# Kernel optimization log

Measured on AMD Instinct MI355X. Metric: run time of the kernel, lower is better.

The kernel has to match this reference:

```python
import jax, jax.numpy as jnp
import numpy as np

LN_EPS = 1e-5


def layer_norm(x, g, b):
    m = jnp.mean(x, axis=-1, keepdims=True)
    v = jnp.mean((x - m) ** 2, axis=-1, keepdims=True)
    return (x - m) * jax.lax.rsqrt(v + LN_EPS) * g + b


def setup_inputs() -> dict:
    key = jax.random.key(0)
    ks = jax.random.split(key, 8)
    B, S, D, C = 32, 512, 768, 25
    return {
        "bert_feature": jax.random.normal(ks[0], (B, S, D), dtype=jnp.float32),
        "output_encoder": jax.random.normal(ks[1], (B, S, D), dtype=jnp.float32),
        "cos_sim": jax.random.normal(ks[2], (B, S, C), dtype=jnp.float32),
        "decoder_embedding": jax.random.normal(ks[3], (B, C, D), dtype=jnp.float32),
        "labels": jax.random.randint(ks[4], (B, S), 0, C, dtype=jnp.int32),
        "ln_gamma": jnp.ones((D,), dtype=jnp.float32),
        "ln_beta": jnp.zeros((D,), dtype=jnp.float32),
        "W_add": jax.random.normal(ks[5], (D, C), dtype=jnp.float32) * 0.02,
        "b_add": jnp.zeros((C,), dtype=jnp.float32),
        "start_trans": jax.random.normal(ks[6], (C,), dtype=jnp.float32) * 0.1,
        "end_trans": jax.random.normal(ks[7], (C,), dtype=jnp.float32) * 0.1,
        "trans": jax.random.normal(jax.random.fold_in(key, 99), (C, C), dtype=jnp.float32) * 0.1,
    }


def crf_neg_log_likelihood(emissions, tags, start, end, trans):
    # emissions [B,S,C] (log-probs), tags [B,S]; no mask (all valid), torchcrf semantics
    B, S, C = emissions.shape
    b = jnp.arange(B)
    # numerator (gold path score)
    em_sc = jnp.take_along_axis(emissions, tags[:, :, None], axis=2)[..., 0].sum(axis=1)
    tr_sc = trans[tags[:, :-1], tags[:, 1:]].sum(axis=1)
    num = start[tags[:, 0]] + em_sc + tr_sc + end[tags[:, -1]]
    # partition function via forward algorithm (scan over time)
    def step(score, em_t):  # score [B,C]
        ns = jax.nn.logsumexp(score[:, :, None] + trans[None] + em_t[:, None, :], axis=1)
        return ns, None
    score0 = start[None] + emissions[:, 0]
    scoreT, _ = jax.lax.scan(step, score0, jnp.swapaxes(emissions[:, 1:], 0, 1))
    logZ = jax.nn.logsumexp(scoreT + end[None], axis=1)
    llh = num - logZ
    return llh.mean()  # reduction='mean'


def crf_decode(emissions, start, end, trans):
    # Viterbi; emissions [B,S,C]
    B, S, C = emissions.shape
    def vstep(score, em_t):
        cand = score[:, :, None] + trans[None]      # [B, prev, cur]
        best = jnp.max(cand, axis=1) + em_t
        idx = jnp.argmax(cand, axis=1)              # [B, cur] -> best prev tag
        return best, idx
    score0 = start[None] + emissions[:, 0]
    scoreT, hist = jax.lax.scan(vstep, score0, jnp.swapaxes(emissions[:, 1:], 0, 1))
    last = jnp.argmax(scoreT + end[None], axis=1)   # [B]
    def back(tag, h):
        prev = jnp.take_along_axis(h, tag[:, None], axis=1)[:, 0]
        return prev, prev
    _, prevs = jax.lax.scan(back, last, hist, reverse=True)
    return jnp.concatenate([prevs, last[None]], axis=0).T  # [B,S]


def reference(bert_feature, output_encoder, cos_sim, decoder_embedding, labels,
              ln_gamma, ln_beta, W_add, b_add, start_trans, end_trans, trans):
    # dropout is identity at eval time
    bf = layer_norm(bert_feature, ln_gamma, ln_beta)
    # prob_times_query: triple python loop == bmm(cos_sim, LN(decoder_embedding))
    # NOTE: original (faithfully) passes raw cos_sim, not its softmax.
    dec = layer_norm(decoder_embedding, ln_gamma, ln_beta)
    prob_query = jnp.einsum('bsc,bcd->bsd', cos_sim, dec)
    emb = layer_norm(bf + output_encoder + prob_query, ln_gamma, ln_beta)
    emb = jax.nn.relu(emb)
    ner_prob = jax.nn.log_softmax(emb @ W_add + b_add, axis=-1)  # [B,S,C]
    cos_sim_prob = jax.nn.softmax(cos_sim, axis=-1)
    llh = crf_neg_log_likelihood(ner_prob, labels, start_trans, end_trans, trans)
    loss = -llh  # model returns -1 * crf_loss
    path = crf_decode(cos_sim_prob, start_trans, end_trans, trans)
    return loss, path
```

## Files before the change

### kernel.cpp

```cpp
#include <hip/hip_runtime.h>
#include <hip/hip_bf16.h>


#define NEGINF (-1e30f)

__device__ __forceinline__ float rlane(float x, int i) {
  return __int_as_float(__builtin_amdgcn_readlane(__float_as_int(x), i));
}
__device__ __forceinline__ float rfl(float x) {
  return __int_as_float(__builtin_amdgcn_readfirstlane(__float_as_int(x)));
}
template <int CTRL, int RMASK>
__device__ __forceinline__ float dppAdd(float x) {
  return x + __int_as_float(__builtin_amdgcn_update_dpp(
                 0, __float_as_int(x), CTRL, RMASK, 0xF, true));
}
__device__ __forceinline__ float wsum(float v) {
  v = dppAdd<0x111, 0xF>(v);
  v = dppAdd<0x112, 0xF>(v);
  v = dppAdd<0x114, 0xF>(v);
  v = dppAdd<0x118, 0xF>(v);
  v = dppAdd<0x142, 0xA>(v);
  v = dppAdd<0x143, 0xC>(v);
  return rlane(v, 63);
}
__device__ __forceinline__ ushort f2bf(float x) {
  __hip_bfloat16 h = __float2bfloat16(x);
  return *reinterpret_cast<ushort*>(&h);
}
__device__ __forceinline__ void ld12(float* x, const float* p, int lane) {
#pragma unroll
  for (int k = 0; k < 3; k++) {
    float4 v = *(const float4*)(p + (lane + (k << 6)) * 4);
    x[4 * k + 0] = v.x; x[4 * k + 1] = v.y; x[4 * k + 2] = v.z; x[4 * k + 3] = v.w;
  }
}
__device__ __forceinline__ void ld12bf(float* x, const ushort* row, int lane) {
  uint2 d0 = *(const uint2*)((const char*)row + lane * 8);
  uint2 d1 = *(const uint2*)((const char*)row + lane * 8 + 512);
  uint2 d2 = *(const uint2*)((const char*)row + lane * 8 + 1024);
  x[0]  = __uint_as_float(d0.x << 16); x[1]  = __uint_as_float(d0.x & 0xffff0000u);
  x[2]  = __uint_as_float(d0.y << 16); x[3]  = __uint_as_float(d0.y & 0xffff0000u);
  x[4]  = __uint_as_float(d1.x << 16); x[5]  = __uint_as_float(d1.x & 0xffff0000u);
  x[6]  = __uint_as_float(d1.y << 16); x[7]  = __uint_as_float(d1.y & 0xffff0000u);
  x[8]  = __uint_as_float(d2.x << 16); x[9]  = __uint_as_float(d2.x & 0xffff0000u);
  x[10] = __uint_as_float(d2.y << 16); x[11] = __uint_as_float(d2.y & 0xffff0000u);
}

__device__ __forceinline__ float max25(const float c[25]) {
  float m0 = fmaxf(fmaxf(c[0], c[1]), c[2]);
  float m1 = fmaxf(fmaxf(c[3], c[4]), c[5]);
  float m2 = fmaxf(fmaxf(c[6], c[7]), c[8]);
  float m3 = fmaxf(fmaxf(c[9], c[10]), c[11]);
  float m4 = fmaxf(fmaxf(c[12], c[13]), c[14]);
  float m5 = fmaxf(fmaxf(c[15], c[16]), c[17]);
  float m6 = fmaxf(fmaxf(c[18], c[19]), c[20]);
  float m7 = fmaxf(fmaxf(c[21], c[22]), c[23]);
  float n0 = fmaxf(fmaxf(m0, m1), m2);
  float n1 = fmaxf(fmaxf(m3, m4), m5);
  float n2 = fmaxf(fmaxf(m6, m7), c[24]);
  return fmaxf(fmaxf(n0, n1), n2);
}

__device__ __forceinline__ void argmax25(const float c[25], float& bv, int& bi) {
  float v[13]; int x[13];
#pragma unroll
  for (int i = 0; i < 12; i++) {
    bool t = c[2 * i + 1] > c[2 * i];
    v[i] = t ? c[2 * i + 1] : c[2 * i];
    x[i] = t ? 2 * i + 1 : 2 * i;
  }
  v[12] = c[24]; x[12] = 24;
  float w[7]; int y[7];
#pragma unroll
  for (int i = 0; i < 6; i++) {
    bool t = v[2 * i + 1] > v[2 * i];
    w[i] = t ? v[2 * i + 1] : v[2 * i];
    y[i] = t ? x[2 * i + 1] : x[2 * i];
  }
  w[6] = v[12]; y[6] = x[12];
  float u[4]; int z[4];
#pragma unroll
  for (int i = 0; i < 3; i++) {
    bool t = w[2 * i + 1] > w[2 * i];
    u[i] = t ? w[2 * i + 1] : w[2 * i];
    z[i] = t ? y[2 * i + 1] : y[2 * i];
  }
  u[3] = w[6]; z[3] = y[6];
  bool t0 = u[1] > u[0]; float a = t0 ? u[1] : u[0]; int ai = t0 ? z[1] : z[0];
  bool t1 = u[3] > u[2]; float b = t1 ? u[3] : u[2]; int bj = t1 ? z[3] : z[2];
  bool t2 = b > a; bv = t2 ? b : a; bi = t2 ? bj : ai;
}

__global__ __launch_bounds__(256) void prep_kernel(
    const float* __restrict__ decemb, const float* __restrict__ gamma,
    const float* __restrict__ beta, const float* __restrict__ Wadd,
    const float* __restrict__ cosim,
    ushort* __restrict__ decb, ushort* __restrict__ wtb, float* __restrict__ csp) {
  const int blk = blockIdx.x;
  const int tid = threadIdx.x;
  __shared__ float sa[4], sq[4];
  __shared__ float sem[12800];
  if (blk < 800) {
    const float* in = decemb + (size_t)blk * 768;
    float x0 = in[tid], x1 = in[tid + 256], x2 = in[tid + 512];
    float s = x0 + x1 + x2, q = x0 * x0 + x1 * x1 + x2 * x2;
    float ws_ = wsum(s), wq = wsum(q);
    int w = tid >> 6, ln = tid & 63;
    if (ln == 0) { sa[w] = ws_; sq[w] = wq; }
    __syncthreads();
    float s1 = sa[0] + sa[1] + sa[2] + sa[3];
    float s2 = sq[0] + sq[1] + sq[2] + sq[3];
    float mean = s1 * (1.f / 768.f);
    float rstd = rsqrtf(s2 * (1.f / 768.f) - mean * mean + 1e-5f);
    ushort* o = decb + (size_t)blk * 768;
    o[tid]       = f2bf((x0 - mean) * rstd * gamma[tid]       + beta[tid]);
    o[tid + 256] = f2bf((x1 - mean) * rstd * gamma[tid + 256] + beta[tid + 256]);
    o[tid + 512] = f2bf((x2 - mean) * rstd * gamma[tid + 512] + beta[tid + 512]);
  } else if (blk < 832) {
    int gid = (blk - 800) * 256 + tid;
    for (int e = gid; e < 19200; e += 32 * 256) {
      int d = e / 25, j = e - d * 25;
      wtb[j * 768 + d] = f2bf(Wadd[e]);
    }
  } else {
    const int b = blk - 832;
    const float4* cb4 = (const float4*)(cosim + (size_t)b * 12800);
    float4* em4 = (float4*)sem;
    for (int i = tid; i < 3200; i += 256) em4[i] = cb4[i];
    __syncthreads();
#pragma unroll
    for (int rr = 0; rr < 2; rr++) {
      const int r = tid + (rr << 8);
      float v[25];
#pragma unroll
      for (int k = 0; k < 25; k++) v[k] = sem[r * 25 + k];
      float m01 = v[0];
#pragma unroll
      for (int k = 1; k < 25; k++) m01 = fmaxf(m01, v[k]);
      float s = 0.f;
#pragma unroll
      for (int k = 0; k < 25; k++) { v[k] = __expf(v[k] - m01); s += v[k]; }
      float rinv = __builtin_amdgcn_rcpf(s);
#pragma unroll
      for (int k = 0; k < 25; k++) sem[r * 25 + k] = v[k] * rinv;
    }
    __syncthreads();
    float4* cp4 = (float4*)(csp + (size_t)b * 12800);
    for (int i = tid; i < 3200; i += 256) cp4[i] = em4[i];
  }
}

__global__ __launch_bounds__(256) void main_kernel(
    const float* __restrict__ bert, const float* __restrict__ oenc,
    const float* __restrict__ cosim, const float* __restrict__ gamma,
    const float* __restrict__ beta, const float* __restrict__ badd,
    const ushort* __restrict__ decb, const ushort* __restrict__ wtb,
    const float* __restrict__ csp, const float* __restrict__ startt,
    const float* __restrict__ endt, const float* __restrict__ trans,
    float* __restrict__ nprob, float* __restrict__ traceF,
    float* __restrict__ traceB, float* __restrict__ out) {
  __shared__ ushort sh[19200];
  const int tid = threadIdx.x;
  const int lane = tid & 63;
  const int wid = tid >> 6;
  const int bid = blockIdx.x;

  if (bid < 64) {
    const bool isFwd = bid < 32;
    const int b = isFwd ? bid : bid - 32;
    const int tl = (lane < 25) ? lane : 24;
    float* em = (float*)sh;
    {
      const float4* src4 = (const float4*)(csp + (size_t)b * 12800 + (isFwd ? 0 : 6300));
      float4* dst4 = (float4*)em;
#pragma unroll
      for (int i = 0; i < 7; i++) {
        int e = tid + (i << 8);
        if (e < 1625) dst4[e] = src4[e];
      }
    }
    __syncthreads();
    if (wid != 0) return;

    if (isFwd) {
      float* tf = traceF + (size_t)b * 16448;
      float Tc[25];
#pragma unroll
      for (int i = 0; i < 25; i++) Tc[i] = trans[i * 25 + tl];
      float sc = startt[tl] + em[tl];
      tf[lane] = sc;
      float emA = em[25 + tl], emB = em[50 + tl];
      for (int t = 1; t <= 256; t++) {
        float emC = em[(t + 2) * 25 + tl];
        float s[25], c[25];
#pragma unroll
        for (int i = 0; i < 25; i++) s[i] = rlane(sc, i);
#pragma unroll
        for (int i = 0; i < 25; i++) c[i] = s[i] + Tc[i];
        float bv = max25(c);
        sc = bv + emA;
        tf[t * 64 + lane] = sc;
        emA = emB; emB = emC;
      }
    } else {
      float* tb = traceB + (size_t)b * 16448;
      float Tr[25];
#pragma unroll
      for (int j = 0; j < 25; j++) Tr[j] = trans[tl * 25 + j];
      float bwd = endt[tl];
      float emA = em[(511 - 252) * 25 + tl], emB = em[(510 - 252) * 25 + tl];
      for (int t = 511; t >= 257; t--) {
        float emC = em[(t - 2 - 252) * 25 + tl];
        tb[(511 - t) * 64 + lane] = bwd;
        float u = bwd + emA;
        float s[25], c[25];
#pragma unroll
        for (int j = 0; j < 25; j++) s[j] = rlane(u, j);
#pragma unroll
        for (int j = 0; j < 25; j++) c[j] = s[j] + Tr[j];
        float bv = max25(c);
        bwd = bv;
        emA = emB; emB = emC;
      }
      tb[255 * 64 + lane] = bwd;
    }
    return;
  }

  if (bid == 64 && tid == 0) out[0] = 0.f;
  const int idx = bid - 64;
  const int swz = (idx & 7) * 256 + (idx >> 3);
  const int b = swz >> 6;
  const int rowg = b * 512 + ((swz & 63) << 3) + (wid << 1);

  {
    const uint4* src = (const uint4*)(decb + (size_t)b * 19200);
    uint4* dst = (uint4*)sh;
#pragma unroll
    for (int i = 0; i < 10; i++) {
      int e = tid + (i << 8);
      if (e < 2400) dst[e] = src[e];
    }
  }
  float g[12], bbv[12];
  ld12(g, gamma, lane);
  ld12(bbv, beta, lane);
  float acc[2][12];
  ld12(acc[0], bert + (size_t)(rowg + 0) * 768, lane);
  ld12(acc[1], bert + (size_t)(rowg + 1) * 768, lane);
  float cs0 = (lane < 25) ? cosim[(size_t)(rowg + 0) * 25 + lane] : 0.f;
  float cs1 = (lane < 25) ? cosim[(size_t)(rowg + 1) * 25 + lane] : 0.f;
  __syncthreads();

#pragma unroll
  for (int r = 0; r < 2; r++) {
    float s = 0.f, q = 0.f;
#pragma unroll
    for (int e = 0; e < 12; e++) { s += acc[r][e]; q += acc[r][e] * acc[r][e]; }
    s = wsum(s); q = wsum(q);
    float mean = s * (1.f / 768.f);
    float rstd = rsqrtf(q * (1.f / 768.f) - mean * mean + 1e-5f);
#pragma unroll
    for (int e = 0; e < 12; e++) acc[r][e] = (acc[r][e] - mean) * rstd * g[e] + bbv[e];
  }

  const char* sd = (const char*)sh;
#pragma unroll 5
  for (int c = 0; c < 25; c++) {
    uint2 d0 = *(const uint2*)(sd + c * 1536 + lane * 8);
    uint2 d1 = *(const uint2*)(sd + c * 1536 + lane * 8 + 512);
    uint2 d2 = *(const uint2*)(sd + c * 1536 + lane * 8 + 1024);
    float dv[12];
    dv[0]  = __uint_as_float(d0.x << 16); dv[1]  = __uint_as_float(d0.x & 0xffff0000u);
    dv[2]  = __uint_as_float(d0.y << 16); dv[3]  = __uint_as_float(d0.y & 0xffff0000u);
    dv[4]  = __uint_as_float(d1.x << 16); dv[5]  = __uint_as_float(d1.x & 0xffff0000u);
    dv[6]  = __uint_as_float(d1.y << 16); dv[7]  = __uint_as_float(d1.y & 0xffff0000u);
    dv[8]  = __uint_as_float(d2.x << 16); dv[9]  = __uint_as_float(d2.x & 0xffff0000u);
    dv[10] = __uint_as_float(d2.y << 16); dv[11] = __uint_as_float(d2.y & 0xffff0000u);
    float f0 = rlane(cs0, c), f1 = rlane(cs1, c);
#pragma unroll
    for (int e = 0; e < 12; e++) {
      acc[0][e] = fmaf(f0, dv[e], acc[0][e]);
      acc[1][e] = fmaf(f1, dv[e], acc[1][e]);
    }
  }

#pragma unroll
  for (int r = 0; r < 2; r++) {
    float y[12];
    ld12(y, oenc + (size_t)(rowg + r) * 768, lane);
#pragma unroll
    for (int e = 0; e < 12; e++) acc[r][e] += y[e];
  }

#pragma unroll
  for (int r = 0; r < 2; r++) {
    float s = 0.f, q = 0.f;
#pragma unroll
    for (int e = 0; e < 12; e++) { s += acc[r][e]; q += acc[r][e] * acc[r][e]; }
    s = wsum(s); q = wsum(q);
    float mean = s * (1.f / 768.f);
    float rstd = rsqrtf(q * (1.f / 768.f) - mean * mean + 1e-5f);
#pragma unroll
    for (int e = 0; e < 12; e++)
      acc[r][e] = fmaxf((acc[r][e] - mean) * rstd * g[e] + bbv[e], 0.f);
  }

  __syncthreads();

  ushort* scw0 = sh + wid * 3400;
  ushort* scw1 = scw0 + 1700;
#pragma unroll 5
  for (int j = 0; j < 25; j++) {
    float wv[12];
    ld12bf(wv, wtb + j * 768, lane);
    float p0 = 0.f, p1 = 0.f;
#pragma unroll
    for (int e = 0; e < 12; e++) {
      p0 = fmaf(acc[0][e], wv[e], p0);
      p1 = fmaf(acc[1][e], wv[e], p1);
    }
    scw0[j * 68 + lane] = f2bf(p0);
    scw1[j * 68 + lane] = f2bf(p1);
  }
  float bav = (lane < 25) ? badd[lane] : 0.f;
  const int jj = (lane < 25) ? lane : 24;
#pragma unroll
  for (int r = 0; r < 2; r++) {
    const ushort* scw = (r == 0) ? scw0 : scw1;
    float lg = bav;
#pragma unroll
    for (int i = 0; i < 16; i++) {
      uint2 u = *(const uint2*)(scw + jj * 68 + i * 4);
      lg += __uint_as_float(u.x << 16);
      lg += __uint_as_float(u.x & 0xffff0000u);
      lg += __uint_as_float(u.y << 16);
      lg += __uint_as_float(u.y & 0xffff0000u);
    }
    float v = (lane < 25) ? lg : NEGINF;
    float m = rfl(lg);
    float e = __expf(v - m);
    float s = wsum(e);
    if (lane < 25) nprob[(size_t)(rowg + r) * 25 + lane] = e * __builtin_amdgcn_rcpf(s);
  }
}

__global__ __launch_bounds__(256) void scan_kernel(
    const float* __restrict__ nprob, const float* __restrict__ csp,
    const float* __restrict__ traceF, const float* __restrict__ traceB,
    const int* __restrict__ labels, const float* __restrict__ startt,
    const float* __restrict__ endt, const float* __restrict__ trans,
    float* __restrict__ out) {
  const int tid = threadIdx.x, lane = tid & 63, wid = tid >> 6;
  const int blk = blockIdx.x;
  const int tl = (lane < 25) ? lane : 24;
  __shared__ __align__(16) unsigned char shraw[13568];

  if (blk < 32) {
    const int b = blk;
    const float* np = nprob + (size_t)b * 12800;
    float* fp = (float*)shraw;
    float* fq = fp + 32;
    float* snum = fq + 32;
    int* sKf = (int*)(snum + 1);
    int* sKb = sKf + 1;
    if (wid == 0) {
      float Mc[25];
#pragma unroll
      for (int i = 0; i < 25; i++) Mc[i] = __expf(trans[i * 25 + tl]);
      float p = (lane < 25) ? __expf(startt[lane]) * np[lane] : 0.f;
      float eA = np[25 + tl], eB = np[50 + tl];
      int K = 0;
      for (int t = 1; t <= 256; t++) {
        float eC = np[(t + 2) * 25 + tl];
        float s[25];
#pragma unroll
        for (int i = 0; i < 25; i++) s[i] = rlane(p, i);
        float a0 = 0, a1 = 0, a2 = 0, a3 = 0, a4 = 0;
#pragma unroll
        for (int i = 0; i < 25; i += 5) {
          a0 = fmaf(s[i + 0], Mc[i + 0], a0);
          a1 = fmaf(s[i + 1], Mc[i + 1], a1);
          a2 = fmaf(s[i + 2], Mc[i + 2], a2);
          a3 = fmaf(s[i + 3], Mc[i + 3], a3);
          a4 = fmaf(s[i + 4], Mc[i + 4], a4);
        }
        float acc = ((a0 + a1) + (a2 + a3)) + a4;
        if ((t & 7) == 0) {
          unsigned mu = 0;
#pragma unroll
          for (int i = 0; i < 25; i++) {
            unsigned ub = __float_as_uint(s[i]);
            mu = (ub > mu) ? ub : mu;
          }
          int e8 = (int)((mu >> 23) & 0xFF);
          acc *= __uint_as_float((unsigned)(254 - e8) << 23);
          K += 127 - e8;
        }
        p = (lane < 25) ? acc * eA : 0.f;
        eA = eB; eB = eC;
      }
      if (lane < 25) fp[lane] = p;
      if (lane == 0) *sKf = K;
    } else if (wid == 1) {
      float MrE[25];
#pragma unroll
      for (int j = 0; j < 25; j++) MrE[j] = __expf(trans[tl * 25 + j]);
      float q = (lane < 25) ? __expf(endt[lane]) : 0.f;
      float eA = np[511 * 25 + tl], eB = np[510 * 25 + tl];
      int K = 0;
      for (int t = 511; t >= 257; t--) {
        float eC = np[(t - 2) * 25 + tl];
        float u = q * eA;
        float s[25];
#pragma unroll
        for (int j = 0; j < 25; j++) s[j] = rlane(u, j);
        float a0 = 0, a1 = 0, a2 = 0, a3 = 0, a4 = 0;
#pragma unroll
        for (int j = 0; j < 25; j += 5) {
          a0 = fmaf(s[j + 0], MrE[j + 0], a0);
          a1 = fmaf(s[j + 1], MrE[j + 1], a1);
          a2 = fmaf(s[j + 2], MrE[j + 2], a2);
          a3 = fmaf(s[j + 3], MrE[j + 3], a3);
          a4 = fmaf(s[j + 4], MrE[j + 4], a4);
        }
        float acc = ((a0 + a1) + (a2 + a3)) + a4;
        if ((t & 7) == 0) {
          unsigned mu = 0;
#pragma unroll
          for (int j = 0; j < 25; j++) {
            unsigned ub = __float_as_uint(s[j]);
            mu = (ub > mu) ? ub : mu;
          }
          int e8 = (int)((mu >> 23) & 0xFF);
          acc *= __uint_as_float((unsigned)(254 - e8) << 23);
          K += 127 - e8;
        }
        q = (lane < 25) ? acc : 0.f;
        eA = eB; eB = eC;
      }
      if (lane < 25) fq[lane] = q;
      if (lane == 0) *sKb = K;
    } else if (wid == 2) {
      float a = 0.f;
      const int* lb = labels + b * 512;
      for (int t = lane; t < 512; t += 64) a += __logf(np[t * 25 + lb[t]]);
      for (int t = lane; t < 511; t += 64) a += trans[lb[t] * 25 + lb[t + 1]];
      a = wsum(a);
      if (lane == 0) *snum = a + startt[lb[0]] + endt[lb[511]];
    }
    __syncthreads();
    if (wid == 0) {
      float z = (lane < 25) ? fp[lane] * fq[lane] : 0.f;
      z = wsum(z);
      float logZ = __logf(z) - (float)(*sKf + *sKb) * 0.6931471805599453f;
      float llh = *snum - logZ;
      if (lane == 0) atomicAdd(out, -llh * (1.f / 32.f));
    }
    return;
  }

  const int vb = blk - 32;
  const int b = vb & 31;
  const bool isFwd = vb < 32;
  unsigned char* hist = shraw;
  const float* tf = traceF + (size_t)b * 16448;
  const float* tb = traceB + (size_t)b * 16448;

  if (isFwd) {
    float Tc[25];
#pragma unroll
    for (int i = 0; i < 25; i++) Tc[i] = trans[i * 25 + tl];
    int t0 = 1 + (wid << 6);
    float vA = tf[(t0 - 1) * 64 + tl];
    for (int n = 0; n < 64; n++) {
      int t = t0 + n;
      float vB = (n < 63) ? tf[t * 64 + tl] : 0.f;
      float s[25], c[25];
#pragma unroll
      for (int i = 0; i < 25; i++) s[i] = rlane(vA, i);
#pragma unroll
      for (int i = 0; i < 25; i++) c[i] = s[i] + Tc[i];
      float bv; int bi;
      argmax25(c, bv, bi);
      if (lane < 25) hist[t * 26 + lane] = (unsigned char)bi;
      vA = vB;
    }
  } else {
    float Tr[25];
#pragma unroll
    for (int j = 0; j < 25; j++) Tr[j] = trans[tl * 25 + j];
    const float* cb = csp + (size_t)b * 12800;
    int t0 = 257 + (wid << 6);
    float tA = (t0 <= 511) ? tb[(511 - t0) * 64 + tl] : 0.f;
    float eA = (t0 <= 511) ? cb[t0 * 25 + tl] : 0.f;
    for (int n = 0; n < 64; n++) {
      int t = t0 + n;
      if (t > 511) break;
      float tBn = (t < 511) ? tb[(511 - t - 1) * 64 + tl] : 0.f;
      float eBn = (t < 511) ? cb[(t + 1) * 25 + tl] : 0.f;
      float u = tA + eA;
      float s[25], c[25];
#pragma unroll
      for (int j = 0; j < 25; j++) s[j] = rlane(u, j);
#pragma unroll
      for (int j = 0; j < 25; j++) c[j] = s[j] + Tr[j];
      float bv; int bj;
      argmax25(c, bv, bj);
      if (lane < 25) hist[t * 26 + lane] = (unsigned char)bj;
      tA = tBn; eA = eBn;
    }
  }
  __syncthreads();
  if (wid == 0) {
    float fv = (lane < 25) ? tf[256 * 64 + lane] + tb[255 * 64 + lane] : NEGINF;
    int idx = lane;
#pragma unroll
    for (int m = 32; m >= 1; m >>= 1) {
      float ov = __shfl_xor(fv, m); int oi = __shfl_xor(idx, m);
      if (ov > fv || (ov == fv && oi < idx)) { fv = ov; idx = oi; }
    }
    int cur = idx;
    float* path = out + 1 + (size_t)b * 512;
    if (isFwd) {
      if (lane == 0) path[256] = (float)cur;
      int h = (lane < 25) ? hist[256 * 26 + lane] : 0;
      for (int t = 256; t >= 1; t--) {
        int hn = (t > 1 && lane < 25) ? hist[(t - 1) * 26 + lane] : 0;
        int prev = __builtin_amdgcn_readlane(h, cur);
        if (lane == 0) path[t - 1] = (float)prev;
        cur = prev; h = hn;
      }
    } else {
      int h = (lane < 25) ? hist[257 * 26 + lane] : 0;
      for (int t = 257; t <= 511; t++) {
        int hn = (t < 511 && lane < 25) ? hist[(t + 1) * 26 + lane] : 0;
        int nx = __builtin_amdgcn_readlane(h, cur);
        if (lane == 0) path[t] = (float)nx;
        cur = nx; h = hn;
      }
    }
  }
}

extern "C" void kernel_launch(void* const* d_in, const int* in_sizes, int n_in,
                              void* d_out, int out_size, void* d_ws, size_t ws_size,
                              hipStream_t stream) {
  (void)in_sizes; (void)n_in; (void)out_size; (void)ws_size;
  const float* bert   = (const float*)d_in[0];
  const float* oenc   = (const float*)d_in[1];
  const float* cosim  = (const float*)d_in[2];
  const float* decemb = (const float*)d_in[3];
  const int*   labels = (const int*)d_in[4];
  const float* gamma  = (const float*)d_in[5];
  const float* beta   = (const float*)d_in[6];
  const float* Wadd   = (const float*)d_in[7];
  const float* badd   = (const float*)d_in[8];
  const float* startt = (const float*)d_in[9];
  const float* endt   = (const float*)d_in[10];
  const float* trans  = (const float*)d_in[11];
  float* out = (float*)d_out;
  char*  wsb = (char*)d_ws;
  ushort* decb   = (ushort*)wsb;
  ushort* wtb    = (ushort*)(wsb + 1228800);
  float*  nprob  = (float*)(wsb + 1305600);
  float*  csp    = (float*)(wsb + 2944000);
  float*  traceF = (float*)(wsb + 4582400);
  float*  traceB = (float*)(wsb + 6687744);

  prep_kernel<<<864, 256, 0, stream>>>(decemb, gamma, beta, Wadd, cosim, decb, wtb, csp);
  main_kernel<<<2112, 256, 0, stream>>>(bert, oenc, cosim, gamma, beta, badd, decb, wtb,
                                        csp, startt, endt, trans, nprob, traceF, traceB, out);
  scan_kernel<<<96, 256, 0, stream>>>(nprob, csp, traceF, traceB, labels, startt, endt,
                                      trans, out);
}
```

Measured before the change: 107.4 us.

## Merge Viterbi forward/backward sweeps into one block and read decoder embedding from global

The forward and backward Viterbi max-plus sweeps, previously run in separate blocks, now interleave inside a single wavefront per batch. The emission table is stored in LDS as bf16 so the whole sequence fits, which changes precision (the scan kernel applies matching bf16 rounding for consistency). The main path no longer stages the decoder embedding into LDS and instead reads it directly from global memory, dropping two block barriers and shrinking shared memory. The aim is fewer blocks, lower LDS use, and two independent dependency chains to hide latency, at the cost of bf16 rounding of the emission scores and uncached global reads.

```diff
diff --git a/kernel.cpp b/kernel.cpp
--- a/kernel.cpp
+++ b/kernel.cpp
@@ -27,6 +27,9 @@
 __device__ __forceinline__ ushort f2bf(float x) {
   __hip_bfloat16 h = __float2bfloat16(x);
   return *reinterpret_cast<ushort*>(&h);
+}
+__device__ __forceinline__ float bfr(float x) {
+  return __uint_as_float((uint)f2bf(x) << 16);
 }
 __device__ __forceinline__ void ld12(float* x, const float* p, int lane) {
 #pragma unroll
@@ -160,89 +163,78 @@
     const float* __restrict__ endt, const float* __restrict__ trans,
     float* __restrict__ nprob, float* __restrict__ traceF,
     float* __restrict__ traceB, float* __restrict__ out) {
-  __shared__ ushort sh[19200];
+  __shared__ ushort sh[13600];
   const int tid = threadIdx.x;
   const int lane = tid & 63;
   const int wid = tid >> 6;
   const int bid = blockIdx.x;
 
-  if (bid < 64) {
-    const bool isFwd = bid < 32;
-    const int b = isFwd ? bid : bid - 32;
+  if (bid < 32) {
+    const int b = bid;
     const int tl = (lane < 25) ? lane : 24;
-    float* em = (float*)sh;
+    ushort* embf = sh;
     {
-      const float4* src4 = (const float4*)(csp + (size_t)b * 12800 + (isFwd ? 0 : 6300));
-      float4* dst4 = (float4*)em;
-#pragma unroll
-      for (int i = 0; i < 7; i++) {
+      const float4* src4 = (const float4*)(csp + (size_t)b * 12800);
+      uint2* dst = (uint2*)sh;
+#pragma unroll
+      for (int i = 0; i < 13; i++) {
         int e = tid + (i << 8);
-        if (e < 1625) dst4[e] = src4[e];
+        if (e < 3200) {
+          float4 v = src4[e];
+          uint2 u;
+          u.x = (uint)f2bf(v.x) | ((uint)f2bf(v.y) << 16);
+          u.y = (uint)f2bf(v.z) | ((uint)f2bf(v.w) << 16);
+          dst[e] = u;
+        }
       }
     }
     __syncthreads();
     if (wid != 0) return;
 
-    if (isFwd) {
-      float* tf = traceF + (size_t)b * 16448;
-      float Tc[25];
-#pragma unroll
-      for (int i = 0; i < 25; i++) Tc[i] = trans[i * 25 + tl];
-      float sc = startt[tl] + em[tl];
-      tf[lane] = sc;
-      float emA = em[25 + tl], emB = em[50 + tl];
-      for (int t = 1; t <= 256; t++) {
-        float emC = em[(t + 2) * 25 + tl];
-        float s[25], c[25];
-#pragma unroll
-        for (int i = 0; i < 25; i++) s[i] = rlane(sc, i);
-#pragma unroll
-        for (int i = 0; i < 25; i++) c[i] = s[i] + Tc[i];
-        float bv = max25(c);
-        sc = bv + emA;
-        tf[t * 64 + lane] = sc;
-        emA = emB; emB = emC;
-      }
-    } else {
-      float* tb = traceB + (size_t)b * 16448;
-      float Tr[25];
-#pragma unroll
-      for (int j = 0; j < 25; j++) Tr[j] = trans[tl * 25 + j];
-      float bwd = endt[tl];
-      float emA = em[(511 - 252) * 25 + tl], emB = em[(510 - 252) * 25 + tl];
-      for (int t = 511; t >= 257; t--) {
-        float emC = em[(t - 2 - 252) * 25 + tl];
-        tb[(511 - t) * 64 + lane] = bwd;
-        float u = bwd + emA;
-        float s[25], c[25];
-#pragma unroll
-        for (int j = 0; j < 25; j++) s[j] = rlane(u, j);
-#pragma unroll
-        for (int j = 0; j < 25; j++) c[j] = s[j] + Tr[j];
-        float bv = max25(c);
-        bwd = bv;
-        emA = emB; emB = emC;
-      }
-      tb[255 * 64 + lane] = bwd;
-    }
+    float* tf = traceF + (size_t)b * 16448;
+    float* tb = traceB + (size_t)b * 16448;
+    float Tc[25], Tr[25];
+#pragma unroll
+    for (int i = 0; i < 25; i++) Tc[i] = trans[i * 25 + tl];
+#pragma unroll
+    for (int j = 0; j < 25; j++) Tr[j] = trans[tl * 25 + j];
+#define EMLD(t) __uint_as_float((uint)embf[(t) * 25 + tl] << 16)
+    float scF = startt[tl] + EMLD(0);
+    tf[lane] = scF;
+    float fA = EMLD(1), fB = EMLD(2);
+    float scB = endt[tl];
+    float bA = EMLD(511), bB = EMLD(510);
+    for (int k = 1; k <= 256; k++) {
+      float fC = EMLD(k + 2);
+      float bC = EMLD(510 - k);
+      tb[(k - 1) * 64 + lane] = scB;
+      float sF[25], cF[25], sB[25], cB[25];
+#pragma unroll
+      for (int i = 0; i < 25; i++) sF[i] = rlane(scF, i);
+#pragma unroll
+      for (int i = 0; i < 25; i++) sB[i] = rlane(scB + bA, i);
+#pragma unroll
+      for (int i = 0; i < 25; i++) cF[i] = sF[i] + Tc[i];
+#pragma unroll
+      for (int i = 0; i < 25; i++) cB[i] = sB[i] + Tr[i];
+      float bvF = max25(cF);
+      float bvB = max25(cB);
+      scF = bvF + fA;
+      scB = bvB;
+      tf[k * 64 + lane] = scF;
+      fA = fB; fB = fC;
+      bA = bB; bB = bC;
+    }
+#undef EMLD
     return;
   }
 
-  if (bid == 64 && tid == 0) out[0] = 0.f;
-  const int idx = bid - 64;
+  if (bid == 32 && tid == 0) out[0] = 0.f;
+  const int idx = bid - 32;
   const int swz = (idx & 7) * 256 + (idx >> 3);
   const int b = swz >> 6;
   const int rowg = b * 512 + ((swz & 63) << 3) + (wid << 1);
 
-  {
-    const uint4* src = (const uint4*)(decb + (size_t)b * 19200);
-    uint4* dst = (uint4*)sh;
-#pragma unroll
-    for (int i = 0; i < 10; i++) {
-      int e = tid + (i << 8);
-      if (e < 2400) dst[e] = src[e];
-    }
-  }
   float g[12], bbv[12];
   ld12(g, gamma, lane);
   ld12(bbv, beta, lane);
@@ -251,7 +243,6 @@
   ld12(acc[1], bert + (size_t)(rowg + 1) * 768, lane);
   float cs0 = (lane < 25) ? cosim[(size_t)(rowg + 0) * 25 + lane] : 0.f;
   float cs1 = (lane < 25) ? cosim[(size_t)(rowg + 1) * 25 + lane] : 0.f;
-  __syncthreads();
 
 #pragma unroll
   for (int r = 0; r < 2; r++) {
@@ -265,19 +256,11 @@
     for (int e = 0; e < 12; e++) acc[r][e] = (acc[r][e] - mean) * rstd * g[e] + bbv[e];
   }
 
-  const char* sd = (const char*)sh;
+  const ushort* db = decb + (size_t)b * 19200;
 #pragma unroll 5
   for (int c = 0; c < 25; c++) {
-    uint2 d0 = *(const uint2*)(sd + c * 1536 + lane * 8);
-    uint2 d1 = *(const uint2*)(sd + c * 1536 + lane * 8 + 512);
-    uint2 d2 = *(const uint2*)(sd + c * 1536 + lane * 8 + 1024);
     float dv[12];
-    dv[0]  = __uint_as_float(d0.x << 16); dv[1]  = __uint_as_float(d0.x & 0xffff0000u);
-    dv[2]  = __uint_as_float(d0.y << 16); dv[3]  = __uint_as_float(d0.y & 0xffff0000u);
-    dv[4]  = __uint_as_float(d1.x << 16); dv[5]  = __uint_as_float(d1.x & 0xffff0000u);
-    dv[6]  = __uint_as_float(d1.y << 16); dv[7]  = __uint_as_float(d1.y & 0xffff0000u);
-    dv[8]  = __uint_as_float(d2.x << 16); dv[9]  = __uint_as_float(d2.x & 0xffff0000u);
-    dv[10] = __uint_as_float(d2.y << 16); dv[11] = __uint_as_float(d2.y & 0xffff0000u);
+    ld12bf(dv, db + c * 768, lane);
     float f0 = rlane(cs0, c), f1 = rlane(cs1, c);
 #pragma unroll
     for (int e = 0; e < 12; e++) {
@@ -306,8 +289,6 @@
     for (int e = 0; e < 12; e++)
       acc[r][e] = fmaxf((acc[r][e] - mean) * rstd * g[e] + bbv[e], 0.f);
   }
-
-  __syncthreads();
 
   ushort* scw0 = sh + wid * 3400;
   ushort* scw1 = scw0 + 1700;
@@ -494,12 +475,12 @@
     const float* cb = csp + (size_t)b * 12800;
     int t0 = 257 + (wid << 6);
     float tA = (t0 <= 511) ? tb[(511 - t0) * 64 + tl] : 0.f;
-    float eA = (t0 <= 511) ? cb[t0 * 25 + tl] : 0.f;
+    float eA = (t0 <= 511) ? bfr(cb[t0 * 25 + tl]) : 0.f;
     for (int n = 0; n < 64; n++) {
       int t = t0 + n;
       if (t > 511) break;
       float tBn = (t < 511) ? tb[(511 - t - 1) * 64 + tl] : 0.f;
-      float eBn = (t < 511) ? cb[(t + 1) * 25 + tl] : 0.f;
+      float eBn = (t < 511) ? bfr(cb[(t + 1) * 25 + tl]) : 0.f;
       float u = tA + eA;
       float s[25], c[25];
 #pragma unroll
@@ -570,7 +551,7 @@
   float*  traceB = (float*)(wsb + 6687744);
 
   prep_kernel<<<864, 256, 0, stream>>>(decemb, gamma, beta, Wadd, cosim, decb, wtb, csp);
-  main_kernel<<<2112, 256, 0, stream>>>(bert, oenc, cosim, gamma, beta, badd, decb, wtb,
+  main_kernel<<<2080, 256, 0, stream>>>(bert, oenc, cosim, gamma, beta, badd, decb, wtb,
                                         csp, startt, endt, trans, nprob, traceF, traceB, out);
   scan_kernel<<<96, 256, 0, stream>>>(nprob, csp, traceF, traceB, labels, startt, endt,
                                       trans, out);
```

Result: slower. 149.7 us (+39.4%).

## Move Viterbi max-plus scans from main kernel into a separate scan kernel

Applied to the files above, without the earlier changes.

The Viterbi forward and backward max-plus passes move out of the first 64 blocks of the large main kernel. They now run in a new scan1 kernel next to the CRF partition-function blocks, and the Viterbi backtrace becomes its own scan2 kernel. This removes the long serial blocks that could stretch the tail of the main kernel, and the main kernel now launches only its 2048 row blocks. The cost is an extra kernel launch, and the serial Viterbi scans no longer overlap with the LayerNorm and GEMM work.

```diff
diff --git a/kernel.cpp b/kernel.cpp
--- a/kernel.cpp
+++ b/kernel.cpp
@@ -156,81 +156,15 @@
     const float* __restrict__ cosim, const float* __restrict__ gamma,
     const float* __restrict__ beta, const float* __restrict__ badd,
     const ushort* __restrict__ decb, const ushort* __restrict__ wtb,
-    const float* __restrict__ csp, const float* __restrict__ startt,
-    const float* __restrict__ endt, const float* __restrict__ trans,
-    float* __restrict__ nprob, float* __restrict__ traceF,
-    float* __restrict__ traceB, float* __restrict__ out) {
+    float* __restrict__ nprob, float* __restrict__ out) {
   __shared__ ushort sh[19200];
   const int tid = threadIdx.x;
   const int lane = tid & 63;
   const int wid = tid >> 6;
   const int bid = blockIdx.x;
-
-  if (bid < 64) {
-    const bool isFwd = bid < 32;
-    const int b = isFwd ? bid : bid - 32;
-    const int tl = (lane < 25) ? lane : 24;
-    float* em = (float*)sh;
-    {
-      const float4* src4 = (const float4*)(csp + (size_t)b * 12800 + (isFwd ? 0 : 6300));
-      float4* dst4 = (float4*)em;
-#pragma unroll
-      for (int i = 0; i < 7; i++) {
-        int e = tid + (i << 8);
-        if (e < 1625) dst4[e] = src4[e];
-      }
-    }
-    __syncthreads();
-    if (wid != 0) return;
-
-    if (isFwd) {
-      float* tf = traceF + (size_t)b * 16448;
-      float Tc[25];
-#pragma unroll
-      for (int i = 0; i < 25; i++) Tc[i] = trans[i * 25 + tl];
-      float sc = startt[tl] + em[tl];
-      tf[lane] = sc;
-      float emA = em[25 + tl], emB = em[50 + tl];
-      for (int t = 1; t <= 256; t++) {
-        float emC = em[(t + 2) * 25 + tl];
-        float s[25], c[25];
-#pragma unroll
-        for (int i = 0; i < 25; i++) s[i] = rlane(sc, i);
-#pragma unroll
-        for (int i = 0; i < 25; i++) c[i] = s[i] + Tc[i];
-        float bv = max25(c);
-        sc = bv + emA;
-        tf[t * 64 + lane] = sc;
-        emA = emB; emB = emC;
-      }
-    } else {
-      float* tb = traceB + (size_t)b * 16448;
-      float Tr[25];
-#pragma unroll
-      for (int j = 0; j < 25; j++) Tr[j] = trans[tl * 25 + j];
-      float bwd = endt[tl];
-      float emA = em[(511 - 252) * 25 + tl], emB = em[(510 - 252) * 25 + tl];
-      for (int t = 511; t >= 257; t--) {
-        float emC = em[(t - 2 - 252) * 25 + tl];
-        tb[(511 - t) * 64 + lane] = bwd;
-        float u = bwd + emA;
-        float s[25], c[25];
-#pragma unroll
-        for (int j = 0; j < 25; j++) s[j] = rlane(u, j);
-#pragma unroll
-        for (int j = 0; j < 25; j++) c[j] = s[j] + Tr[j];
-        float bv = max25(c);
-        bwd = bv;
-        emA = emB; emB = emC;
-      }
-      tb[255 * 64 + lane] = bwd;
-    }
-    return;
-  }
-
-  if (bid == 64 && tid == 0) out[0] = 0.f;
-  const int idx = bid - 64;
-  const int swz = (idx & 7) * 256 + (idx >> 3);
+  if (bid == 0 && tid == 0) out[0] = 0.f;
+
+  const int swz = (bid & 7) * 256 + (bid >> 3);
   const int b = swz >> 6;
   const int rowg = b * 512 + ((swz & 63) << 3) + (wid << 1);
 
@@ -346,16 +280,16 @@
   }
 }
 
-__global__ __launch_bounds__(256) void scan_kernel(
+__global__ __launch_bounds__(256) void scan1_kernel(
     const float* __restrict__ nprob, const float* __restrict__ csp,
-    const float* __restrict__ traceF, const float* __restrict__ traceB,
     const int* __restrict__ labels, const float* __restrict__ startt,
     const float* __restrict__ endt, const float* __restrict__ trans,
+    float* __restrict__ traceF, float* __restrict__ traceB,
     float* __restrict__ out) {
   const int tid = threadIdx.x, lane = tid & 63, wid = tid >> 6;
   const int blk = blockIdx.x;
   const int tl = (lane < 25) ? lane : 24;
-  __shared__ __align__(16) unsigned char shraw[13568];
+  __shared__ __align__(16) unsigned char shraw[26000];
 
   if (blk < 32) {
     const int b = blk;
@@ -462,9 +396,75 @@
   }
 
   const int vb = blk - 32;
+  const bool isFwd = vb < 32;
+  const int b = isFwd ? vb : vb - 32;
+  float* em = (float*)shraw;
+  {
+    const float4* src4 = (const float4*)(csp + (size_t)b * 12800 + (isFwd ? 0 : 6300));
+    float4* dst4 = (float4*)em;
+#pragma unroll
+    for (int i = 0; i < 7; i++) {
+      int e = tid + (i << 8);
+      if (e < 1625) dst4[e] = src4[e];
+    }
+  }
+  __syncthreads();
+  if (wid != 0) return;
+
+  if (isFwd) {
+    float* tf = traceF + (size_t)b * 16448;
+    float Tc[25];
+#pragma unroll
+    for (int i = 0; i < 25; i++) Tc[i] = trans[i * 25 + tl];
+    float sc = startt[tl] + em[tl];
+    tf[lane] = sc;
+    float emA = em[25 + tl], emB = em[50 + tl];
+    for (int t = 1; t <= 256; t++) {
+      float emC = em[(t + 2) * 25 + tl];
+      float s[25], c[25];
+#pragma unroll
+      for (int i = 0; i < 25; i++) s[i] = rlane(sc, i);
+#pragma unroll
+      for (int i = 0; i < 25; i++) c[i] = s[i] + Tc[i];
+      float bv = max25(c);
+      sc = bv + emA;
+      tf[t * 64 + lane] = sc;
+      emA = emB; emB = emC;
+    }
+  } else {
+    float* tb = traceB + (size_t)b * 16448;
+    float Tr[25];
+#pragma unroll
+    for (int j = 0; j < 25; j++) Tr[j] = trans[tl * 25 + j];
+    float bwd = endt[tl];
+    float emA = em[(511 - 252) * 25 + tl], emB = em[(510 - 252) * 25 + tl];
+    for (int t = 511; t >= 257; t--) {
+      float emC = em[(t - 2 - 252) * 25 + tl];
+      tb[(511 - t) * 64 + lane] = bwd;
+      float u = bwd + emA;
+      float s[25], c[25];
+#pragma unroll
+      for (int j = 0; j < 25; j++) s[j] = rlane(u, j);
+#pragma unroll
+      for (int j = 0; j < 25; j++) c[j] = s[j] + Tr[j];
+      float bv = max25(c);
+      bwd = bv;
+      emA = emB; emB = emC;
+    }
+    tb[255 * 64 + lane] = bwd;
+  }
+}
+
+__global__ __launch_bounds__(256) void scan2_kernel(
+    const float* __restrict__ csp, const float* __restrict__ traceF,
+    const float* __restrict__ traceB, const float* __restrict__ trans,
+    float* __restrict__ out) {
+  const int tid = threadIdx.x, lane = tid & 63, wid = tid >> 6;
+  const int vb = blockIdx.x;
   const int b = vb & 31;
   const bool isFwd = vb < 32;
-  unsigned char* hist = shraw;
+  const int tl = (lane < 25) ? lane : 24;
+  __shared__ __align__(16) unsigned char hist[13568];
   const float* tf = traceF + (size_t)b * 16448;
   const float* tb = traceB + (size_t)b * 16448;
 
@@ -570,8 +570,9 @@
   float*  traceB = (float*)(wsb + 6687744);
 
   prep_kernel<<<864, 256, 0, stream>>>(decemb, gamma, beta, Wadd, cosim, decb, wtb, csp);
-  main_kernel<<<2112, 256, 0, stream>>>(bert, oenc, cosim, gamma, beta, badd, decb, wtb,
-                                        csp, startt, endt, trans, nprob, traceF, traceB, out);
-  scan_kernel<<<96, 256, 0, stream>>>(nprob, csp, traceF, traceB, labels, startt, endt,
-                                      trans, out);
-}
+  main_kernel<<<2048, 256, 0, stream>>>(bert, oenc, cosim, gamma, beta, badd, decb, wtb,
+                                        nprob, out);
+  scan1_kernel<<<96, 256, 0, stream>>>(nprob, csp, labels, startt, endt, trans,
+                                       traceF, traceB, out);
+  scan2_kernel<<<64, 256, 0, stream>>>(csp, traceF, traceB, trans, out);
+}
```

Measured after the change: 129.4 us. +20.5%, slower.

## Process four rows per wave in main kernel, split scan kernel, raise Viterbi priority

Applied to the files above, without the earlier changes.

Each wave in the main kernel now handles four rows instead of two. This halves the grid and amortizes the per-block shared-memory load of the decoder embedding and the per-wave gamma/beta loads over more rows. The Viterbi trace waves raise their scheduling priority with s_setprio while they run alongside the LayerNorm blocks. The old combined scan kernel is split into a CRF-likelihood kernel and a Viterbi backtrack kernel, which adds a launch. Four-row accumulators raise register pressure and may lower occupancy.

```diff
diff --git a/kernel.cpp b/kernel.cpp
--- a/kernel.cpp
+++ b/kernel.cpp
@@ -183,6 +183,7 @@
     __syncthreads();
     if (wid != 0) return;
 
+    __builtin_amdgcn_s_setprio(1);
     if (isFwd) {
       float* tf = traceF + (size_t)b * 16448;
       float Tc[25];
@@ -225,14 +226,15 @@
       }
       tb[255 * 64 + lane] = bwd;
     }
+    __builtin_amdgcn_s_setprio(0);
     return;
   }
 
   if (bid == 64 && tid == 0) out[0] = 0.f;
   const int idx = bid - 64;
-  const int swz = (idx & 7) * 256 + (idx >> 3);
-  const int b = swz >> 6;
-  const int rowg = b * 512 + ((swz & 63) << 3) + (wid << 1);
+  const int swz = (idx & 7) * 128 + (idx >> 3);
+  const int b = swz >> 5;
+  const int rowg = b * 512 + ((swz & 31) << 4) + (wid << 2);
 
   {
     const uint4* src = (const uint4*)(decb + (size_t)b * 19200);
@@ -246,15 +248,17 @@
   float g[12], bbv[12];
   ld12(g, gamma, lane);
   ld12(bbv, beta, lane);
-  float acc[2][12];
-  ld12(acc[0], bert + (size_t)(rowg + 0) * 768, lane);
-  ld12(acc[1], bert + (size_t)(rowg + 1) * 768, lane);
-  float cs0 = (lane < 25) ? cosim[(size_t)(rowg + 0) * 25 + lane] : 0.f;
-  float cs1 = (lane < 25) ? cosim[(size_t)(rowg + 1) * 25 + lane] : 0.f;
+  float acc[4][12];
+#pragma unroll
+  for (int r = 0; r < 4; r++) ld12(acc[r], bert + (size_t)(rowg + r) * 768, lane);
+  float cs[4];
+#pragma unroll
+  for (int r = 0; r < 4; r++)
+    cs[r] = (lane < 25) ? cosim[(size_t)(rowg + r) * 25 + lane] : 0.f;
   __syncthreads();
 
 #pragma unroll
-  for (int r = 0; r < 2; r++) {
+  for (int r = 0; r < 4; r++) {
     float s = 0.f, q = 0.f;
 #pragma unroll
     for (int e = 0; e < 12; e++) { s += acc[r][e]; q += acc[r][e] * acc[r][e]; }
@@ -278,16 +282,19 @@
     dv[6]  = __uint_as_float(d1.y << 16); dv[7]  = __uint_as_float(d1.y & 0xffff0000u);
     dv[8]  = __uint_as_float(d2.x << 16); dv[9]  = __uint_as_float(d2.x & 0xffff0000u);
     dv[10] = __uint_as_float(d2.y << 16); dv[11] = __uint_as_float(d2.y & 0xffff0000u);
-    float f0 = rlane(cs0, c), f1 = rlane(cs1, c);
+    float f0 = rlane(cs[0], c), f1 = rlane(cs[1], c);
+    float f2 = rlane(cs[2], c), f3 = rlane(cs[3], c);
 #pragma unroll
     for (int e = 0; e < 12; e++) {
       acc[0][e] = fmaf(f0, dv[e], acc[0][e]);
       acc[1][e] = fmaf(f1, dv[e], acc[1][e]);
-    }
-  }
-
-#pragma unroll
-  for (int r = 0; r < 2; r++) {
+      acc[2][e] = fmaf(f2, dv[e], acc[2][e]);
+      acc[3][e] = fmaf(f3, dv[e], acc[3][e]);
+    }
+  }
+
+#pragma unroll
+  for (int r = 0; r < 4; r++) {
     float y[12];
     ld12(y, oenc + (size_t)(rowg + r) * 768, lane);
 #pragma unroll
@@ -295,7 +302,7 @@
   }
 
 #pragma unroll
-  for (int r = 0; r < 2; r++) {
+  for (int r = 0; r < 4; r++) {
     float s = 0.f, q = 0.f;
 #pragma unroll
     for (int e = 0; e < 12; e++) { s += acc[r][e]; q += acc[r][e] * acc[r][e]; }
@@ -311,160 +318,162 @@
 
   ushort* scw0 = sh + wid * 3400;
   ushort* scw1 = scw0 + 1700;
-#pragma unroll 5
-  for (int j = 0; j < 25; j++) {
-    float wv[12];
-    ld12bf(wv, wtb + j * 768, lane);
-    float p0 = 0.f, p1 = 0.f;
-#pragma unroll
-    for (int e = 0; e < 12; e++) {
-      p0 = fmaf(acc[0][e], wv[e], p0);
-      p1 = fmaf(acc[1][e], wv[e], p1);
-    }
-    scw0[j * 68 + lane] = f2bf(p0);
-    scw1[j * 68 + lane] = f2bf(p1);
-  }
   float bav = (lane < 25) ? badd[lane] : 0.f;
   const int jj = (lane < 25) ? lane : 24;
 #pragma unroll
-  for (int r = 0; r < 2; r++) {
-    const ushort* scw = (r == 0) ? scw0 : scw1;
-    float lg = bav;
-#pragma unroll
-    for (int i = 0; i < 16; i++) {
-      uint2 u = *(const uint2*)(scw + jj * 68 + i * 4);
-      lg += __uint_as_float(u.x << 16);
-      lg += __uint_as_float(u.x & 0xffff0000u);
-      lg += __uint_as_float(u.y << 16);
-      lg += __uint_as_float(u.y & 0xffff0000u);
-    }
-    float v = (lane < 25) ? lg : NEGINF;
-    float m = rfl(lg);
-    float e = __expf(v - m);
-    float s = wsum(e);
-    if (lane < 25) nprob[(size_t)(rowg + r) * 25 + lane] = e * __builtin_amdgcn_rcpf(s);
-  }
-}
-
-__global__ __launch_bounds__(256) void scan_kernel(
-    const float* __restrict__ nprob, const float* __restrict__ csp,
-    const float* __restrict__ traceF, const float* __restrict__ traceB,
-    const int* __restrict__ labels, const float* __restrict__ startt,
-    const float* __restrict__ endt, const float* __restrict__ trans,
+  for (int h = 0; h < 2; h++) {
+    const int r0 = 2 * h, r1 = 2 * h + 1;
+#pragma unroll 5
+    for (int j = 0; j < 25; j++) {
+      float wv[12];
+      ld12bf(wv, wtb + j * 768, lane);
+      float p0 = 0.f, p1 = 0.f;
+#pragma unroll
+      for (int e = 0; e < 12; e++) {
+        p0 = fmaf(acc[r0][e], wv[e], p0);
+        p1 = fmaf(acc[r1][e], wv[e], p1);
+      }
+      scw0[j * 68 + lane] = f2bf(p0);
+      scw1[j * 68 + lane] = f2bf(p1);
+    }
+#pragma unroll
+    for (int r = 0; r < 2; r++) {
+      const ushort* scw = (r == 0) ? scw0 : scw1;
+      float lg = bav;
+#pragma unroll
+      for (int i = 0; i < 16; i++) {
+        uint2 u = *(const uint2*)(scw + jj * 68 + i * 4);
+        lg += __uint_as_float(u.x << 16);
+        lg += __uint_as_float(u.x & 0xffff0000u);
+        lg += __uint_as_float(u.y << 16);
+        lg += __uint_as_float(u.y & 0xffff0000u);
+      }
+      float v = (lane < 25) ? lg : NEGINF;
+      float m = rfl(lg);
+      float e = __expf(v - m);
+      float s = wsum(e);
+      if (lane < 25)
+        nprob[(size_t)(rowg + r0 + r) * 25 + lane] = e * __builtin_amdgcn_rcpf(s);
+    }
+  }
+}
+
+__global__ __launch_bounds__(256) void crf_kernel(
+    const float* __restrict__ nprob, const int* __restrict__ labels,
+    const float* __restrict__ startt, const float* __restrict__ endt,
+    const float* __restrict__ trans, float* __restrict__ out) {
+  const int tid = threadIdx.x, lane = tid & 63, wid = tid >> 6;
+  const int b = blockIdx.x;
+  const int tl = (lane < 25) ? lane : 24;
+  __shared__ float fp[32], fq[32], snum[1];
+  __shared__ int sKf[1], sKb[1];
+  const float* np = nprob + (size_t)b * 12800;
+
+  if (wid == 0) {
+    float Mc[25];
+#pragma unroll
+    for (int i = 0; i < 25; i++) Mc[i] = __expf(trans[i * 25 + tl]);
+    float p = (lane < 25) ? __expf(startt[lane]) * np[lane] : 0.f;
+    float eA = np[25 + tl], eB = np[50 + tl];
+    int K = 0;
+    for (int t = 1; t <= 256; t++) {
+      float eC = np[(t + 2) * 25 + tl];
+      float s[25];
+#pragma unroll
+      for (int i = 0; i < 25; i++) s[i] = rlane(p, i);
+      float a0 = 0, a1 = 0, a2 = 0, a3 = 0, a4 = 0;
+#pragma unroll
+      for (int i = 0; i < 25; i += 5) {
+        a0 = fmaf(s[i + 0], Mc[i + 0], a0);
+        a1 = fmaf(s[i + 1], Mc[i + 1], a1);
+        a2 = fmaf(s[i + 2], Mc[i + 2], a2);
+        a3 = fmaf(s[i + 3], Mc[i + 3], a3);
+        a4 = fmaf(s[i + 4], Mc[i + 4], a4);
+      }
+      float acc = ((a0 + a1) + (a2 + a3)) + a4;
+      if ((t & 7) == 0) {
+        unsigned mu = 0;
+#pragma unroll
+        for (int i = 0; i < 25; i++) {
+          unsigned ub = __float_as_uint(s[i]);
+          mu = (ub > mu) ? ub : mu;
+        }
+        int e8 = (int)((mu >> 23) & 0xFF);
+        acc *= __uint_as_float((unsigned)(254 - e8) << 23);
+        K += 127 - e8;
+      }
+      p = (lane < 25) ? acc * eA : 0.f;
+      eA = eB; eB = eC;
+    }
+    if (lane < 25) fp[lane] = p;
+    if (lane == 0) sKf[0] = K;
+  } else if (wid == 1) {
+    float MrE[25];
+#pragma unroll
+    for (int j = 0; j < 25; j++) MrE[j] = __expf(trans[tl * 25 + j]);
+    float q = (lane < 25) ? __expf(endt[lane]) : 0.f;
+    float eA = np[511 * 25 + tl], eB = np[510 * 25 + tl];
+    int K = 0;
+    for (int t = 511; t >= 257; t--) {
+      float eC = np[(t - 2) * 25 + tl];
+      float u = q * eA;
+      float s[25];
+#pragma unroll
+      for (int j = 0; j < 25; j++) s[j] = rlane(u, j);
+      float a0 = 0, a1 = 0, a2 = 0, a3 = 0, a4 = 0;
+#pragma unroll
+      for (int j = 0; j < 25; j += 5) {
+        a0 = fmaf(s[j + 0], MrE[j + 0], a0);
+        a1 = fmaf(s[j + 1], MrE[j + 1], a1);
+        a2 = fmaf(s[j + 2], MrE[j + 2], a2);
+        a3 = fmaf(s[j + 3], MrE[j + 3], a3);
+        a4 = fmaf(s[j + 4], MrE[j + 4], a4);
+      }
+      float acc = ((a0 + a1) + (a2 + a3)) + a4;
+      if ((t & 7) == 0) {
+        unsigned mu = 0;
+#pragma unroll
+        for (int j = 0; j < 25; j++) {
+          unsigned ub = __float_as_uint(s[j]);
+          mu = (ub > mu) ? ub : mu;
+        }
+        int e8 = (int)((mu >> 23) & 0xFF);
+        acc *= __uint_as_float((unsigned)(254 - e8) << 23);
+        K += 127 - e8;
+      }
+      q = (lane < 25) ? acc : 0.f;
+      eA = eB; eB = eC;
+    }
+    if (lane < 25) fq[lane] = q;
+    if (lane == 0) sKb[0] = K;
+  } else if (wid == 2) {
+    float a = 0.f;
+    const int* lb = labels + b * 512;
+    for (int t = lane; t < 512; t += 64) a += __logf(np[t * 25 + lb[t]]);
+    for (int t = lane; t < 511; t += 64) a += trans[lb[t] * 25 + lb[t + 1]];
+    a = wsum(a);
+    if (lane == 0) snum[0] = a + startt[lb[0]] + endt[lb[511]];
+  }
+  __syncthreads();
+  if (wid == 0) {
+    float z = (lane < 25) ? fp[lane] * fq[lane] : 0.f;
+    z = wsum(z);
+    float logZ = __logf(z) - (float)(sKf[0] + sKb[0]) * 0.6931471805599453f;
+    float llh = snum[0] - logZ;
+    if (lane == 0) atomicAdd(out, -llh * (1.f / 32.f));
+  }
+}
+
+__global__ __launch_bounds__(256) void scan2_kernel(
+    const float* __restrict__ csp, const float* __restrict__ traceF,
+    const float* __restrict__ traceB, const float* __restrict__ trans,
     float* __restrict__ out) {
   const int tid = threadIdx.x, lane = tid & 63, wid = tid >> 6;
-  const int blk = blockIdx.x;
-  const int tl = (lane < 25) ? lane : 24;
-  __shared__ __align__(16) unsigned char shraw[13568];
-
-  if (blk < 32) {
-    const int b = blk;
-    const float* np = nprob + (size_t)b * 12800;
-    float* fp = (float*)shraw;
-    float* fq = fp + 32;
-    float* snum = fq + 32;
-    int* sKf = (int*)(snum + 1);
-    int* sKb = sKf + 1;
-    if (wid == 0) {
-      float Mc[25];
-#pragma unroll
-      for (int i = 0; i < 25; i++) Mc[i] = __expf(trans[i * 25 + tl]);
-      float p = (lane < 25) ? __expf(startt[lane]) * np[lane] : 0.f;
-      float eA = np[25 + tl], eB = np[50 + tl];
-      int K = 0;
-      for (int t = 1; t <= 256; t++) {
-        float eC = np[(t + 2) * 25 + tl];
-        float s[25];
-#pragma unroll
-        for (int i = 0; i < 25; i++) s[i] = rlane(p, i);
-        float a0 = 0, a1 = 0, a2 = 0, a3 = 0, a4 = 0;
-#pragma unroll
-        for (int i = 0; i < 25; i += 5) {
-          a0 = fmaf(s[i + 0], Mc[i + 0], a0);
-          a1 = fmaf(s[i + 1], Mc[i + 1], a1);
-          a2 = fmaf(s[i + 2], Mc[i + 2], a2);
-          a3 = fmaf(s[i + 3], Mc[i + 3], a3);
-          a4 = fmaf(s[i + 4], Mc[i + 4], a4);
-        }
-        float acc = ((a0 + a1) + (a2 + a3)) + a4;
-        if ((t & 7) == 0) {
-          unsigned mu = 0;
-#pragma unroll
-          for (int i = 0; i < 25; i++) {
-            unsigned ub = __float_as_uint(s[i]);
-            mu = (ub > mu) ? ub : mu;
-          }
-          int e8 = (int)((mu >> 23) & 0xFF);
-          acc *= __uint_as_float((unsigned)(254 - e8) << 23);
-          K += 127 - e8;
-        }
-        p = (lane < 25) ? acc * eA : 0.f;
-        eA = eB; eB = eC;
-      }
-      if (lane < 25) fp[lane] = p;
-      if (lane == 0) *sKf = K;
-    } else if (wid == 1) {
-      float MrE[25];
-#pragma unroll
-      for (int j = 0; j < 25; j++) MrE[j] = __expf(trans[tl * 25 + j]);
-      float q = (lane < 25) ? __expf(endt[lane]) : 0.f;
-      float eA = np[511 * 25 + tl], eB = np[510 * 25 + tl];
-      int K = 0;
-      for (int t = 511; t >= 257; t--) {
-        float eC = np[(t - 2) * 25 + tl];
-        float u = q * eA;
-        float s[25];
-#pragma unroll
-        for (int j = 0; j < 25; j++) s[j] = rlane(u, j);
-        float a0 = 0, a1 = 0, a2 = 0, a3 = 0, a4 = 0;
-#pragma unroll
-        for (int j = 0; j < 25; j += 5) {
-          a0 = fmaf(s[j + 0], MrE[j + 0], a0);
-          a1 = fmaf(s[j + 1], MrE[j + 1], a1);
-          a2 = fmaf(s[j + 2], MrE[j + 2], a2);
-          a3 = fmaf(s[j + 3], MrE[j + 3], a3);
-          a4 = fmaf(s[j + 4], MrE[j + 4], a4);
-        }
-        float acc = ((a0 + a1) + (a2 + a3)) + a4;
-        if ((t & 7) == 0) {
-          unsigned mu = 0;
-#pragma unroll
-          for (int j = 0; j < 25; j++) {
-            unsigned ub = __float_as_uint(s[j]);
-            mu = (ub > mu) ? ub : mu;
-          }
-          int e8 = (int)((mu >> 23) & 0xFF);
-          acc *= __uint_as_float((unsigned)(254 - e8) << 23);
-          K += 127 - e8;
-        }
-        q = (lane < 25) ? acc : 0.f;
-        eA = eB; eB = eC;
-      }
-      if (lane < 25) fq[lane] = q;
-      if (lane == 0) *sKb = K;
-    } else if (wid == 2) {
-      float a = 0.f;
-      const int* lb = labels + b * 512;
-      for (int t = lane; t < 512; t += 64) a += __logf(np[t * 25 + lb[t]]);
-      for (int t = lane; t < 511; t += 64) a += trans[lb[t] * 25 + lb[t + 1]];
-      a = wsum(a);
-      if (lane == 0) *snum = a + startt[lb[0]] + endt[lb[511]];
-    }
-    __syncthreads();
-    if (wid == 0) {
-      float z = (lane < 25) ? fp[lane] * fq[lane] : 0.f;
-      z = wsum(z);
-      float logZ = __logf(z) - (float)(*sKf + *sKb) * 0.6931471805599453f;
-      float llh = *snum - logZ;
-      if (lane == 0) atomicAdd(out, -llh * (1.f / 32.f));
-    }
-    return;
-  }
-
-  const int vb = blk - 32;
+  const int vb = blockIdx.x;
   const int b = vb & 31;
   const bool isFwd = vb < 32;
-  unsigned char* hist = shraw;
+  const int tl = (lane < 25) ? lane : 24;
+  __shared__ __align__(16) unsigned char hist[13568];
   const float* tf = traceF + (size_t)b * 16448;
   const float* tb = traceB + (size_t)b * 16448;
 
@@ -570,8 +579,8 @@
   float*  traceB = (float*)(wsb + 6687744);
 
   prep_kernel<<<864, 256, 0, stream>>>(decemb, gamma, beta, Wadd, cosim, decb, wtb, csp);
-  main_kernel<<<2112, 256, 0, stream>>>(bert, oenc, cosim, gamma, beta, badd, decb, wtb,
+  main_kernel<<<1088, 256, 0, stream>>>(bert, oenc, cosim, gamma, beta, badd, decb, wtb,
                                         csp, startt, endt, trans, nprob, traceF, traceB, out);
-  scan_kernel<<<96, 256, 0, stream>>>(nprob, csp, traceF, traceB, labels, startt, endt,
-                                      trans, out);
-}
+  crf_kernel<<<32, 256, 0, stream>>>(nprob, labels, startt, endt, trans, out);
+  scan2_kernel<<<64, 256, 0, stream>>>(csp, traceF, traceB, trans, out);
+}
```

Measured after the change: 144.6 us. 1.35x slower.
